# Optimization experiments

Measured on AMD Instinct MI355X. Metric: run time of the kernel, lower is better.

The kernel has to match this reference:

```python
import jax, jax.numpy as jnp
import numpy as np

N_EMBED = 1024
N_HEADS = 16
HEAD_DIM = N_EMBED // N_HEADS


def setup_inputs() -> dict:
    key = jax.random.key(0)
    ks = jax.random.split(key, 5)
    x = jax.random.normal(ks[0], (4, 2048, N_EMBED), dtype=jnp.float32)
    # Linear params (torch nn.Linear: y = x @ W.T + b); store W as [in, out]
    s = 1.0 / np.sqrt(N_EMBED)
    W_attn = jax.random.uniform(ks[1], (N_EMBED, 3 * N_EMBED), minval=-s, maxval=s, dtype=jnp.float32)
    b_attn = jax.random.uniform(ks[2], (3 * N_EMBED,), minval=-s, maxval=s, dtype=jnp.float32)
    W_proj = jax.random.uniform(ks[3], (N_EMBED, N_EMBED), minval=-s, maxval=s, dtype=jnp.float32)
    b_proj = jax.random.uniform(ks[4], (N_EMBED,), minval=-s, maxval=s, dtype=jnp.float32)
    return {"x": x, "W_attn": W_attn, "b_attn": b_attn, "W_proj": W_proj, "b_proj": b_proj}


def reference(x, W_attn, b_attn, W_proj, b_proj):
    B, L, D = x.shape
    H, Hd = N_HEADS, HEAD_DIM
    qkv = x @ W_attn + b_attn  # [B, L, 3D]
    q, k, v = jnp.split(qkv, 3, axis=-1)
    q = q.reshape(B, L, H, Hd).transpose(0, 2, 1, 3)  # [B, H, L, Hd]
    k = k.reshape(B, L, H, Hd).transpose(0, 2, 1, 3)
    v = v.reshape(B, L, H, Hd).transpose(0, 2, 1, 3)
    scores = jnp.einsum('bhqd,bhkd->bhqk', q, k) / jnp.sqrt(jnp.float32(Hd))
    causal = jnp.tril(jnp.ones((L, L), dtype=bool))
    scores = jnp.where(causal[None, None], scores, -jnp.inf)
    probs = jax.nn.softmax(scores.astype(jnp.float32), axis=-1).astype(x.dtype)
    o = jnp.einsum('bhqk,bhkd->bhqd', probs, v)  # [B, H, L, Hd]
    o = o.transpose(0, 2, 1, 3).reshape(B, L, D)
    return o @ W_proj + b_proj
```

## Files before the change

kernel.cpp:

```cpp
#include <hip/hip_runtime.h>


typedef __attribute__((ext_vector_type(8))) short short8;
typedef __attribute__((ext_vector_type(4))) short s16x4;
typedef __attribute__((ext_vector_type(4))) float f32x4;

#define DEVI __device__ __forceinline__

constexpr int NE = 1024, NH = 16, NB = 4, L = 2048;
constexpr int M = NB * L;
constexpr int KD = 1024;

DEVI unsigned f2bf(float f) {
    union { float f; unsigned u; } v; v.f = f;
    unsigned u = v.u;
    u += 0x7fffu + ((u >> 16) & 1u);
    return u >> 16;
}
DEVI unsigned pack_bf2(float lo, float hi) {
    union { float f; unsigned u; } a, b; a.f = lo; b.f = hi;
    return ((a.u + 0x8000u) >> 16) | ((b.u + 0x8000u) & 0xffff0000u);
}

typedef const __attribute__((address_space(1))) void* gas_t;
typedef __attribute__((address_space(3))) void* las_t;
DEVI void gl_lds16(const void* g, void* l) {
    __builtin_amdgcn_global_load_lds((gas_t)g, (las_t)l, 16, 0, 0);
}

__global__ void k_f32_to_bf16(const float* __restrict__ in,
                              unsigned short* __restrict__ out, int n8) {
    int i = blockIdx.x * blockDim.x + threadIdx.x;
    if (i >= n8) return;
    const float4* p = (const float4*)in + (size_t)i * 2;
    float4 a = p[0], b = p[1];
    short8 r;
    r[0] = f2bf(a.x); r[1] = f2bf(a.y); r[2] = f2bf(a.z); r[3] = f2bf(a.w);
    r[4] = f2bf(b.x); r[5] = f2bf(b.y); r[6] = f2bf(b.z); r[7] = f2bf(b.w);
    ((short8*)out)[i] = r;
}

__global__ void k_transpose_bf16(const float* __restrict__ in,
                                 unsigned short* __restrict__ out, int R, int C) {
    __shared__ float t[32][33];
    int x = blockIdx.x * 32 + threadIdx.x;
    int y0 = blockIdx.y * 32;
#pragma unroll
    for (int i = 0; i < 4; i++)
        t[threadIdx.y + 8 * i][threadIdx.x] = in[(size_t)(y0 + threadIdx.y + 8 * i) * C + x];
    __syncthreads();
    int xo = y0 + threadIdx.x;
    int yo = blockIdx.x * 32 + threadIdx.y;
#pragma unroll
    for (int i = 0; i < 4; i++)
        out[(size_t)(yo + 8 * i) * R + xo] = f2bf(t[threadIdx.x][threadIdx.y + 8 * i]);
}

template <int MODE>
__global__ __launch_bounds__(256, 4)
void k_gemm(const unsigned short* __restrict__ A,
            const unsigned short* __restrict__ Bt,
            const float* __restrict__ bias,
            unsigned short* __restrict__ Qb,
            unsigned short* __restrict__ Kb,
            unsigned short* __restrict__ Vt,
            float* __restrict__ out) {
    __shared__ alignas(16) short As[128 * 64];
    __shared__ alignas(16) short Bs[128 * 64];
    const int tid = threadIdx.x;
    const int lane = tid & 63, wid = tid >> 6;
    const int quad = lane >> 4, l16 = lane & 15;
    const int wm = (wid >> 1) * 64, wn = (wid & 1) * 64;
    const int m0 = blockIdx.y * 128;
    const int n0 = blockIdx.x * 128;

    const int srow = lane >> 3;
    const int gseg = (lane & 7) ^ srow;

    f32x4 acc[4][4] = {};

    for (int kk = 0; kk < KD; kk += 64) {
        __syncthreads();
#pragma unroll
        for (int c = 0; c < 4; c++) {
            const int rbase = c * 32 + wid * 8;
            gl_lds16(&A[(size_t)(m0 + rbase + srow) * KD + kk + gseg * 8], &As[rbase * 64]);
            gl_lds16(&Bt[(size_t)(n0 + rbase + srow) * KD + kk + gseg * 8], &Bs[rbase * 64]);
        }
        __syncthreads();
#pragma unroll
        for (int kc = 0; kc < 2; kc++) {
            short8 af[4], bf[4];
#pragma unroll
            for (int t = 0; t < 4; t++) {
                const int Ra = wm + t * 16 + l16;
                af[t] = *(const short8*)&As[Ra * 64 + (((kc * 4 + quad) ^ (Ra & 7)) * 8)];
                const int Rb = wn + t * 16 + l16;
                bf[t] = *(const short8*)&Bs[Rb * 64 + (((kc * 4 + quad) ^ (Rb & 7)) * 8)];
            }
#pragma unroll
            for (int mt = 0; mt < 4; mt++)
#pragma unroll
                for (int nt = 0; nt < 4; nt++)
                    acc[mt][nt] = __builtin_amdgcn_mfma_f32_16x16x32_bf16(
                        af[mt], bf[nt], acc[mt][nt], 0, 0, 0);
        }
    }

#pragma unroll
    for (int nt = 0; nt < 4; nt++) {
        const int n = n0 + wn + nt * 16 + l16;
        const float bv = bias[n];
        if (MODE == 0) {
            const int sel = n >> 10;
            const int h = (n & 1023) >> 6;
            const int d = n & 63;
#pragma unroll
            for (int mt = 0; mt < 4; mt++)
#pragma unroll
                for (int r = 0; r < 4; r++) {
                    const int m = m0 + wm + mt * 16 + quad * 4 + r;
                    const int b = m >> 11, l = m & 2047;
                    const int bh = b * NH + h;
                    const float v = acc[mt][nt][r] + bv;
                    if (sel == 0)      Qb[(size_t)(bh * L + l) * 64 + d] = f2bf(v * 0.125f);
                    else if (sel == 1) Kb[(size_t)(bh * L + l) * 64 + d] = f2bf(v);
                    else               Vt[(size_t)(bh * 64 + d) * L + l] = f2bf(v);
                }
        } else {
#pragma unroll
            for (int mt = 0; mt < 4; mt++)
#pragma unroll
                for (int r = 0; r < 4; r++) {
                    const int m = m0 + wm + mt * 16 + quad * 4 + r;
                    out[(size_t)m * NE + n] = acc[mt][nt][r] + bv;
                }
        }
    }
}

__global__ __launch_bounds__(256, 4)
void k_attn(const unsigned short* __restrict__ Q,
            const unsigned short* __restrict__ Kb,
            const unsigned short* __restrict__ Vt,
            unsigned short* __restrict__ O) {
    __shared__ alignas(16) short smem[16384];
    short* Ks = smem;
    short* Vs = smem + 8192;
    short* Os = smem;

    const int tid = threadIdx.x;
    const int lane = tid & 63, wid = tid >> 6;
    const int quad = lane >> 4, l16 = lane & 15;
    const int bh = blockIdx.x;
    const int qb = 15 - (int)blockIdx.y;
    const int q0 = qb * 128 + wid * 32;
    const size_t base = (size_t)bh * L * 64;
    const int b = bh >> 4, h = bh & 15;

    const int srowK = lane >> 3;
    const int gsegK = (lane & 7) ^ srowK;
    const int vrow_off = (lane >> 4);
    const int vseg = lane & 15;

    short8 qf[2][2];
#pragma unroll
    for (int mt = 0; mt < 2; mt++)
#pragma unroll
        for (int dc = 0; dc < 2; dc++)
            qf[mt][dc] = *(const short8*)&Q[base + (size_t)(q0 + mt * 16 + l16) * 64 + dc * 32 + quad * 8];

    f32x4 o[2][4] = {};
    float lrow[2] = {0.f, 0.f};

    for (int kt = 0; kt <= qb; kt++) {
        __syncthreads();
#pragma unroll
        for (int c = 0; c < 4; c++) {
            const int rbase = c * 32 + wid * 8;
            gl_lds16(&Kb[base + (size_t)(kt * 128 + rbase + srowK) * 64 + gsegK * 8],
                     &Ks[rbase * 64]);
        }
#pragma unroll
        for (int c = 0; c < 4; c++) {
            const int rbase = c * 16 + wid * 4;
            const int row = rbase + vrow_off;
            const int gs = vseg ^ (row & 15);
            gl_lds16(&Vt[base + (size_t)row * L + kt * 128 + gs * 8], &Vs[rbase * 128]);
        }
        __syncthreads();

        const bool diag = (kt == qb);
        const int chunks = diag ? (wid + 1) : 4;

        for (int kc = 0; kc < chunks; kc++) {
            short8 kf[2][2];
#pragma unroll
            for (int j0 = 0; j0 < 2; j0++)
#pragma unroll
                for (int dc = 0; dc < 2; dc++) {
                    const int R = kc * 32 + j0 * 16 + l16;
                    kf[j0][dc] = *(const short8*)&Ks[R * 64 + (((dc * 4 + quad) ^ (R & 7)) * 8)];
                }
            f32x4 st[2][2];
#pragma unroll
            for (int mt = 0; mt < 2; mt++)
#pragma unroll
                for (int j0 = 0; j0 < 2; j0++) {
                    f32x4 z = {};
                    z = __builtin_amdgcn_mfma_f32_16x16x32_bf16(kf[j0][0], qf[mt][0], z, 0, 0, 0);
                    z = __builtin_amdgcn_mfma_f32_16x16x32_bf16(kf[j0][1], qf[mt][1], z, 0, 0, 0);
                    st[mt][j0] = z;
                }
            const bool dm = diag && (kc == wid);
            short8 pb[2];
#pragma unroll
            for (int mt = 0; mt < 2; mt++) {
                float pe[8];
                float sum = 0.f;
#pragma unroll
                for (int j0 = 0; j0 < 2; j0++)
#pragma unroll
                    for (int r = 0; r < 4; r++) {
                        float p = __expf(st[mt][j0][r]);
                        if (dm) {
                            const int krel = j0 * 16 + quad * 4 + r;
                            const int qrel = mt * 16 + l16;
                            if (krel > qrel) p = 0.f;
                        }
                        sum += p;
                        pe[j0 * 4 + r] = p;
                    }
                lrow[mt] += sum;
#pragma unroll
                for (int w = 0; w < 4; w++) {
                    unsigned pk = pack_bf2(pe[2 * w], pe[2 * w + 1]);
                    pb[mt][2 * w] = (short)(pk & 0xffff);
                    pb[mt][2 * w + 1] = (short)(pk >> 16);
                }
            }
#pragma unroll
            for (int dt = 0; dt < 4; dt++) {
                const int R2 = dt * 16 + l16;
                const int s16a = kc * 4 + (quad >> 1);
                const int off = (quad & 1) * 4;
                s16x4 lo = *(const s16x4*)&Vs[R2 * 128 + ((s16a ^ l16) * 8) + off];
                s16x4 hi = *(const s16x4*)&Vs[R2 * 128 + (((s16a + 2) ^ l16) * 8) + off];
                short8 vf = __builtin_shufflevector(lo, hi, 0, 1, 2, 3, 4, 5, 6, 7);
#pragma unroll
                for (int mt = 0; mt < 2; mt++)
                    o[mt][dt] = __builtin_amdgcn_mfma_f32_16x16x32_bf16(
                        vf, pb[mt], o[mt][dt], 0, 0, 0);
            }
        }
    }

    float inv[2];
#pragma unroll
    for (int mt = 0; mt < 2; mt++) {
        float rs = lrow[mt];
        rs += __shfl_xor(rs, 16);
        rs += __shfl_xor(rs, 32);
        inv[mt] = 1.0f / rs;
    }

    __syncthreads();
#pragma unroll
    for (int mt = 0; mt < 2; mt++) {
        const int ql = wid * 32 + mt * 16 + l16;
#pragma unroll
        for (int dt = 0; dt < 4; dt++) {
            unsigned w0 = f2bf(o[mt][dt][0] * inv[mt]) | (f2bf(o[mt][dt][1] * inv[mt]) << 16);
            unsigned w1 = f2bf(o[mt][dt][2] * inv[mt]) | (f2bf(o[mt][dt][3] * inv[mt]) << 16);
            *(uint2*)&Os[ql * 72 + dt * 16 + quad * 4] = make_uint2(w0, w1);
        }
    }
    __syncthreads();
#pragma unroll
    for (int i = 0; i < 4; i++) {
        const int id = i * 256 + tid;
        const int row = id >> 3, seg = id & 7;
        short8 v = *(const short8*)&Os[row * 72 + seg * 8];
        const int q = qb * 128 + row;
        *(short8*)&O[(size_t)(b * L + q) * NE + h * 64 + seg * 8] = v;
    }
}

extern "C" void kernel_launch(void* const* d_in, const int* in_sizes, int n_in,
                              void* d_out, int out_size, void* d_ws, size_t ws_size,
                              hipStream_t stream) {
    const float* x  = (const float*)d_in[0];
    const float* Wa = (const float*)d_in[1];
    const float* ba = (const float*)d_in[2];
    const float* Wp = (const float*)d_in[3];
    const float* bp = (const float*)d_in[4];
    float* out = (float*)d_out;

    char* ws = (char*)d_ws;
    unsigned short* xb  = (unsigned short*)(ws);
    unsigned short* WaT = (unsigned short*)(ws + (16u << 20));
    unsigned short* WpT = (unsigned short*)(ws + (22u << 20));
    unsigned short* Qb  = (unsigned short*)(ws + (24u << 20));
    unsigned short* Kb  = (unsigned short*)(ws + (40u << 20));
    unsigned short* Vt  = (unsigned short*)(ws + (56u << 20));

    k_f32_to_bf16<<<(M * NE / 8 + 255) / 256, 256, 0, stream>>>(x, xb, M * NE / 8);
    k_transpose_bf16<<<dim3(3 * NE / 32, NE / 32), dim3(32, 8), 0, stream>>>(Wa, WaT, NE, 3 * NE);
    k_transpose_bf16<<<dim3(NE / 32, NE / 32), dim3(32, 8), 0, stream>>>(Wp, WpT, NE, NE);

    k_gemm<0><<<dim3(3 * NE / 128, M / 128), 256, 0, stream>>>(xb, WaT, ba, Qb, Kb, Vt, nullptr);

    unsigned short* Ob = xb;
    k_attn<<<dim3(NB * NH, 16), 256, 0, stream>>>(Qb, Kb, Vt, Ob);

    k_gemm<1><<<dim3(NE / 128, M / 128), 256, 0, stream>>>(Ob, WpT, bp, nullptr, nullptr, nullptr, out);
}
```

Baseline: 257.8 us.

## Replace GEMM with 8-wave 256-row tiles and multi-stage prefetch pipeline

Replaces the simple 128x128 GEMM, which issued a load and then synchronized every k-step, with an 8-wave 512-thread kernel. It uses 256xBN tiles, triple-buffered A and double-buffered B in LDS, and prefetches two k-tiles ahead with fine-grained vmcnt waits and MFMA clusters at raised priority. A block-id swizzle spreads consecutive workgroups across XCDs and tiles for cache reuse. This hides global-to-LDS latency and raises arithmetic intensity, at the cost of much larger LDS use, lower occupancy and delicate hand-counted waitcnt values.

Result: slower. 271.1 us (+5.1%).

```diff
diff --git a/kernel.cpp b/kernel.cpp
--- a/kernel.cpp
+++ b/kernel.cpp
@@ -56,70 +56,154 @@
         out[(size_t)(yo + 8 * i) * R + xo] = f2bf(t[threadIdx.x][threadIdx.y + 8 * i]);
 }
 
+
+#define PH_SYNC                                                      \
+    __builtin_amdgcn_s_barrier();                                    \
+    asm volatile("s_waitcnt lgkmcnt(0)" ::: "memory");               \
+    __builtin_amdgcn_sched_barrier(0);
+
+#define RD_A(ROFF, SWZ)                                              \
+    _Pragma("unroll") for (int mt = 0; mt < 4; mt++)                 \
+        af[mt] = *(const short8*)&aCur[((ROFF) + mt * 16 + l16) * 64 + (SWZ)];
+
+#define RD_B(BF, SWZ)                                                \
+    _Pragma("unroll") for (int nt = 0; nt < NF; nt++)                \
+        BF[nt] = *(const short8*)&bCur[(bro + nt * 16 + l16) * 64 + (SWZ)];
+
+#define MFMA_CLU(MH4, BF)                                            \
+    __builtin_amdgcn_s_setprio(1);                                   \
+    _Pragma("unroll") for (int mt = 0; mt < 4; mt++)                 \
+    _Pragma("unroll") for (int nt = 0; nt < NF; nt++)                \
+        acc[(MH4) + mt][nt] = __builtin_amdgcn_mfma_f32_16x16x32_bf16( \
+            af[mt], BF[nt], acc[(MH4) + mt][nt], 0, 0, 0);           \
+    __builtin_amdgcn_s_setprio(0);
+
+#define GTILE(KT, CA, CA2, PAR, DOPRE)                               \
+  {                                                                  \
+    const short* aCur = &As3[(CA) * 16384 + wg_m * 8192];            \
+    const short* bCur = &Bs[(PAR) * (BN * 64)];                      \
+                                             \
+    RD_A(0, swz0)                                                    \
+    RD_B(bf0, swz0)                                                  \
+    if (DOPRE) stA((KT) + 2, 0, (CA2));                              \
+    PH_SYNC                                                          \
+    MFMA_CLU(0, bf0)                                                 \
+    __builtin_amdgcn_s_barrier();                                    \
+                                             \
+    RD_A(64, swz0)                                                   \
+    if (DOPRE) stA((KT) + 2, 1, (CA2));                              \
+    PH_SYNC                                                          \
+    MFMA_CLU(4, bf0)                                                 \
+    __builtin_amdgcn_s_barrier();                                    \
+                                             \
+    RD_A(0, swz1)                                                    \
+    RD_B(bf1, swz1)                                                  \
+    PH_SYNC                                                          \
+    MFMA_CLU(0, bf1)                                                 \
+    __builtin_amdgcn_s_barrier();                                    \
+                                             \
+    RD_A(64, swz1)                                                   \
+    if (DOPRE) { stB((KT) + 2, 0, (PAR)); stB((KT) + 2, 1, (PAR)); } \
+    PH_SYNC                                                          \
+    MFMA_CLU(4, bf1)                                                 \
+    if (DOPRE) {                                                     \
+        if (MODE == 0) asm volatile("s_waitcnt vmcnt(8)" ::: "memory"); \
+        else           asm volatile("s_waitcnt vmcnt(6)" ::: "memory"); \
+    } else {                                                         \
+        asm volatile("s_waitcnt vmcnt(0)" ::: "memory");             \
+    }                                                                \
+    __builtin_amdgcn_s_barrier();                                    \
+  }
+
 template <int MODE>
-__global__ __launch_bounds__(256, 4)
-void k_gemm(const unsigned short* __restrict__ A,
-            const unsigned short* __restrict__ Bt,
-            const float* __restrict__ bias,
-            unsigned short* __restrict__ Qb,
-            unsigned short* __restrict__ Kb,
-            unsigned short* __restrict__ Vt,
-            float* __restrict__ out) {
-    __shared__ alignas(16) short As[128 * 64];
-    __shared__ alignas(16) short Bs[128 * 64];
+__global__ __launch_bounds__(512, 2)
+void k_gemm8(const unsigned short* __restrict__ A,
+             const unsigned short* __restrict__ Bt,
+             const float* __restrict__ bias,
+             unsigned short* __restrict__ Qb,
+             unsigned short* __restrict__ Kb,
+             unsigned short* __restrict__ Vt,
+             float* __restrict__ out) {
+    constexpr int BN  = (MODE == 0) ? 256 : 128;
+    constexpr int NF  = BN / 64;
+    constexpr int NBN = (MODE == 0) ? 12 : 8;
+    constexpr int NWG = (MODE == 0) ? 384 : 256;
+    constexpr int NT  = KD / 64;
+
+    __shared__ alignas(16) short As3[3 * 2 * 128 * 64];
+    __shared__ alignas(16) short Bs[2 * BN * 64];
+
     const int tid = threadIdx.x;
     const int lane = tid & 63, wid = tid >> 6;
     const int quad = lane >> 4, l16 = lane & 15;
-    const int wm = (wid >> 1) * 64, wn = (wid & 1) * 64;
-    const int m0 = blockIdx.y * 128;
-    const int n0 = blockIdx.x * 128;
+    const int wg_m = wid >> 2, wg_n = wid & 3;
+
+    const int id = ((int)blockIdx.x & 7) * (NWG >> 3) + ((int)blockIdx.x >> 3);
+    const int mb = id / NBN, nb = id - mb * NBN;
+    const int m0 = mb * 256, n0 = nb * BN;
 
     const int srow = lane >> 3;
-    const int gseg = (lane & 7) ^ srow;
-
-    f32x4 acc[4][4] = {};
-
-    for (int kk = 0; kk < KD; kk += 64) {
-        __syncthreads();
-#pragma unroll
-        for (int c = 0; c < 4; c++) {
-            const int rbase = c * 32 + wid * 8;
-            gl_lds16(&A[(size_t)(m0 + rbase + srow) * KD + kk + gseg * 8], &As[rbase * 64]);
-            gl_lds16(&Bt[(size_t)(n0 + rbase + srow) * KD + kk + gseg * 8], &Bs[rbase * 64]);
-        }
-        __syncthreads();
-#pragma unroll
-        for (int kc = 0; kc < 2; kc++) {
-            short8 af[4], bf[4];
-#pragma unroll
-            for (int t = 0; t < 4; t++) {
-                const int Ra = wm + t * 16 + l16;
-                af[t] = *(const short8*)&As[Ra * 64 + (((kc * 4 + quad) ^ (Ra & 7)) * 8)];
-                const int Rb = wn + t * 16 + l16;
-                bf[t] = *(const short8*)&Bs[Rb * 64 + (((kc * 4 + quad) ^ (Rb & 7)) * 8)];
-            }
-#pragma unroll
-            for (int mt = 0; mt < 4; mt++)
-#pragma unroll
-                for (int nt = 0; nt < 4; nt++)
-                    acc[mt][nt] = __builtin_amdgcn_mfma_f32_16x16x32_bf16(
-                        af[mt], bf[nt], acc[mt][nt], 0, 0, 0);
-        }
-    }
-
-#pragma unroll
-    for (int nt = 0; nt < 4; nt++) {
-        const int n = n0 + wn + nt * 16 + l16;
+    const int gcol = ((lane & 7) ^ srow) * 8;
+
+    const unsigned short* Ag = A + (size_t)m0 * KD + gcol;
+    const unsigned short* Bg = Bt + (size_t)n0 * KD + gcol;
+
+    auto stA = [&](int kt, int h, int reg) {
+#pragma unroll
+        for (int c = 0; c < 2; c++) {
+            const int rb = wid * 16 + c * 8;
+            gl_lds16(Ag + (size_t)(h * 128 + rb + srow) * KD + kt * 64,
+                     &As3[reg * 16384 + h * 8192 + rb * 64]);
+        }
+    };
+    auto stB = [&](int kt, int h, int reg) {
+#pragma unroll
+        for (int c = 0; c < BN / 128; c++) {
+            const int rb = wid * (BN / 128) * 8 + c * 8;
+            gl_lds16(Bg + (size_t)(h * (BN / 2) + rb + srow) * KD + kt * 64,
+                     &Bs[reg * (BN * 64) + h * (BN / 2) * 64 + rb * 64]);
+        }
+    };
+
+    const int swz0 = ((quad) ^ (l16 & 7)) * 8;
+    const int swz1 = ((4 + quad) ^ (l16 & 7)) * 8;
+    const int bro = wg_n * (BN / 4);
+
+    f32x4 acc[8][NF] = {};
+    short8 af[4], bf0[NF], bf1[NF];
+
+    stA(0, 0, 0); stA(0, 1, 0);
+    stB(0, 0, 0); stB(0, 1, 0);
+    stA(1, 0, 1); stA(1, 1, 1);
+    stB(1, 0, 1); stB(1, 1, 1);
+    if (MODE == 0) asm volatile("s_waitcnt vmcnt(8)" ::: "memory");
+    else           asm volatile("s_waitcnt vmcnt(6)" ::: "memory");
+    __builtin_amdgcn_s_barrier();
+
+    int ca = 0;
+    for (int kt = 0; kt < NT - 2; kt++) {
+        const int ca2 = (ca >= 1) ? ca - 1 : 2;
+        const int par = kt & 1;
+        GTILE(kt, ca, ca2, par, 1)
+        ca = (ca >= 2) ? 0 : ca + 1;
+    }
+    GTILE(NT - 2, ca, 0, ((NT - 2) & 1), 0)
+    ca = (ca >= 2) ? 0 : ca + 1;
+    GTILE(NT - 1, ca, 0, ((NT - 1) & 1), 0)
+
+#pragma unroll
+    for (int nt = 0; nt < NF; nt++) {
+        const int n = n0 + wg_n * (BN / 4) + nt * 16 + l16;
         const float bv = bias[n];
         if (MODE == 0) {
             const int sel = n >> 10;
             const int h = (n & 1023) >> 6;
             const int d = n & 63;
 #pragma unroll
-            for (int mt = 0; mt < 4; mt++)
+            for (int mt = 0; mt < 8; mt++)
 #pragma unroll
                 for (int r = 0; r < 4; r++) {
-                    const int m = m0 + wm + mt * 16 + quad * 4 + r;
+                    const int m = m0 + wg_m * 128 + mt * 16 + quad * 4 + r;
                     const int b = m >> 11, l = m & 2047;
                     const int bh = b * NH + h;
                     const float v = acc[mt][nt][r] + bv;
@@ -129,10 +213,10 @@
                 }
         } else {
 #pragma unroll
-            for (int mt = 0; mt < 4; mt++)
+            for (int mt = 0; mt < 8; mt++)
 #pragma unroll
                 for (int r = 0; r < 4; r++) {
-                    const int m = m0 + wm + mt * 16 + quad * 4 + r;
+                    const int m = m0 + wg_m * 128 + mt * 16 + quad * 4 + r;
                     out[(size_t)m * NE + n] = acc[mt][nt][r] + bv;
                 }
         }
@@ -308,10 +392,10 @@
     k_transpose_bf16<<<dim3(3 * NE / 32, NE / 32), dim3(32, 8), 0, stream>>>(Wa, WaT, NE, 3 * NE);
     k_transpose_bf16<<<dim3(NE / 32, NE / 32), dim3(32, 8), 0, stream>>>(Wp, WpT, NE, NE);
 
-    k_gemm<0><<<dim3(3 * NE / 128, M / 128), 256, 0, stream>>>(xb, WaT, ba, Qb, Kb, Vt, nullptr);
+    k_gemm8<0><<<dim3(384), 512, 0, stream>>>(xb, WaT, ba, Qb, Kb, Vt, nullptr);
 
     unsigned short* Ob = xb;
     k_attn<<<dim3(NB * NH, 16), 256, 0, stream>>>(Qb, Kb, Vt, Ob);
 
-    k_gemm<1><<<dim3(NE / 128, M / 128), 256, 0, stream>>>(Ob, WpT, bp, nullptr, nullptr, nullptr, out);
-}
+    k_gemm8<1><<<dim3(256), 512, 0, stream>>>(Ob, WpT, bp, nullptr, nullptr, nullptr, out);
+}
```
